# Performance work log

Hardware: AMD Instinct MI355X
Metric: run time of the kernel (lower is better)

Reference implementation:

```python
import jax, jax.numpy as jnp
import numpy as np


def _made_masks(D, H):
    # Standard MADE masks, natural ordering, param_count=2 (shift, log_scale).
    d_in = np.arange(1, D + 1)                      # input degrees 1..D
    d_h = (np.arange(H) % (D - 1)) + 1              # hidden degrees cycle 1..D-1
    d_out = np.tile(d_in, 2)                        # output degrees, 2 params per dim
    M1 = (d_h[None, :] >= d_in[:, None]).astype(np.float32)   # [D, H]
    M2 = (d_out[None, :] > d_h[:, None]).astype(np.float32)
    return jnp.asarray(M1), jnp.asarray(M2)


def setup_inputs() -> dict:
    key = jax.random.key(0)
    B, D, H = 4096, 1024, 4096
    k0, k1, k2 = jax.random.split(key, 3)
    z = jax.random.normal(k0, (B, D), dtype=jnp.float32)
    W1 = jax.random.normal(k1, (D, H), dtype=jnp.float32) * (1.0 / np.sqrt(D))
    b1 = jnp.zeros((H,), dtype=jnp.float32)
    # small init on output layer keeps exp(log_scale) well-conditioned
    W2 = jax.random.normal(k2, (H, 2 * D), dtype=jnp.float32) * (0.1 / np.sqrt(H))
    b2 = jnp.zeros((2 * D,), dtype=jnp.float32)
    permutation = jnp.arange(D, dtype=jnp.int32)
    return {"z": z, "W1": W1, "b1": b1, "W2": W2, "b2": b2, "permutation": permutation}


def reference(z, W1, b1, W2, b2, permutation):
    # IAR.forward_flow: permute -> MADE masked MLP -> split params -> affine transform -> inverse permute
    D = z.shape[1]
    H = W1.shape[1]
    M1, M2 = _made_masks(D, H)
    zp = z[:, permutation]                          # permute_data
    h = jax.nn.relu(zp @ (W1 * M1) + b1)            # [B, H]
    res = h @ (W2 * M2) + b2                        # [B, 2D]
    mu, log_s = res[:, :D], res[:, D:]              # res.split(dim_in, dim=1)
    x = zp * jnp.exp(log_s) + mu                    # affine transform, forward=True
    log_det = jnp.sum(log_s, axis=1)                # [B]
    inv = jnp.argsort(permutation)                  # inv_permute_data
    return x[:, inv], log_det
```

## Files before the change

### kernel.cpp

```cpp
#include <hip/hip_runtime.h>
#include <stdint.h>


typedef float   f32x4  __attribute__((ext_vector_type(4)));
typedef int     i32x4  __attribute__((ext_vector_type(4)));
typedef int     i32x8  __attribute__((ext_vector_type(8)));

__device__ __forceinline__ uint8_t f2fp8(float f) {
    int p = __builtin_amdgcn_cvt_pk_fp8_f32(f, 0.0f, 0, false);
    return (uint8_t)(p & 0xff);
}
__device__ __forceinline__ int8_t f2i8(float v, float s) {
    float q = rintf(v * s);
    q = fminf(fmaxf(q, -127.0f), 127.0f);
    return (int8_t)q;
}

#define GLD16(g, l)                                                          \
    __builtin_amdgcn_global_load_lds(                                        \
        (const __attribute__((address_space(1))) uint32_t*)(g),              \
        (__attribute__((address_space(3))) uint32_t*)(l), 16, 0, 0)

#define MFMA_MX(a, b, c)                                                     \
    __builtin_amdgcn_mfma_scale_f32_16x16x128_f8f6f4(                        \
        (a), (b), (c), 0, 0, 0, 0x7F7F7F7F, 0, 0x7F7F7F7F)

__global__ __launch_bounds__(256) void prep_k(
    const float* __restrict__ W1, int8_t* __restrict__ W1mT,
    const float* __restrict__ W2, uint8_t* __restrict__ W2mT,
    float* __restrict__ ws2p,
    const float* __restrict__ z, const int* __restrict__ perm,
    int8_t* __restrict__ zp, float* __restrict__ ld,
    int D, int H, int B) {
    const int bx  = blockIdx.x;
    const int tid = threadIdx.x;
    const int NB1 = (H / 64) * (D / 64);
    const int NB2 = (2 * D / 64) * (H / 64);

    if (bx < NB1) {
        __shared__ int8_t t[64][68];
        const int c0 = (bx % (H / 64)) * 64;
        const int r0 = (bx / (H / 64)) * 64;
        const int q  = tid & 15;
        const int r  = tid >> 4;

        const int fid = bx * 256 + tid;
        if (fid < B) ld[fid] = 0.0f;

#pragma unroll
        for (int rr0 = 0; rr0 < 64; rr0 += 16) {
            const int rr  = rr0 + r;
            const int row = r0 + rr;
            const float4 v4 =
                *(const float4*)&W1[(size_t)row * H + c0 + q * 4];
            const float vv[4] = {v4.x, v4.y, v4.z, v4.w};
            union { int8_t b4[4]; uint32_t u; } pk;
#pragma unroll
            for (int j = 0; j < 4; j++) {
                const int c = c0 + q * 4 + j;
                pk.b4[j] = ((c % (D - 1)) >= row) ? f2i8(vv[j], 1024.0f)
                                                  : (int8_t)0;
            }
            *(uint32_t*)&t[rr][q * 4] = pk.u;
        }
        __syncthreads();
#pragma unroll
        for (int pass = 0; pass < 2; pass++) {
            const int cc = pass * 32 + (tid >> 3);
            const int j0 = (tid & 7) * 8;
            union { int8_t b[8]; uint64_t qq; } v;
#pragma unroll
            for (int j = 0; j < 8; j++) v.b[j] = t[j0 + j][cc];
            *(uint64_t*)&W1mT[(size_t)(c0 + cc) * D + r0 + j0] = v.qq;
        }
    } else if (bx < NB1 + NB2) {
        __shared__ uint8_t t[64][68];
        const int idx = bx - NB1;
        const int c0 = (idx % (2 * D / 64)) * 64;
        const int r0 = (idx / (2 * D / 64)) * 64;
        const int q  = tid & 15;
        const int r  = tid >> 4;
        const bool second = (c0 >= D);
        const int cb = (c0 - D) >> 6;

#pragma unroll
        for (int rr0 = 0; rr0 < 64; rr0 += 16) {
            const int rr  = rr0 + r;
            const int row = r0 + rr;
            const float4 v4 =
                *(const float4*)&W2[(size_t)row * 2 * D + c0 + q * 4];
            const float vv[4] = {v4.x, v4.y, v4.z, v4.w};
            union { uint8_t b4[4]; uint32_t u; } pk;
            float s = 0.0f;
#pragma unroll
            for (int j = 0; j < 4; j++) {
                const int c = c0 + q * 4 + j;
                const bool keep = ((c % D) > (row % (D - 1)));
                pk.b4[j] = keep ? f2fp8(vv[j] * 256.0f) : (uint8_t)0;
                s += keep ? vv[j] : 0.0f;
            }
            *(uint32_t*)&t[rr][q * 4] = pk.u;
            if (second) {
#pragma unroll
                for (int o = 8; o > 0; o >>= 1) s += __shfl_down(s, o, 16);
                if (q == 0) ws2p[(size_t)cb * H + row] = s;
            }
        }
        __syncthreads();
#pragma unroll
        for (int pass = 0; pass < 2; pass++) {
            const int cc = pass * 32 + (tid >> 3);
            const int j0 = (tid & 7) * 8;
            union { uint8_t b[8]; uint64_t qq; } v;
#pragma unroll
            for (int j = 0; j < 8; j++) v.b[j] = t[j0 + j][cc];
            *(uint64_t*)&W2mT[(size_t)(c0 + cc) * H + r0 + j0] = v.qq;
        }
    } else {
        const int bp = bx - NB1 - NB2;
        const int i0 = tid * 4;
        const int4 p4 = *(const int4*)(perm + i0);
#pragma unroll
        for (int rr = 0; rr < 2; rr++) {
            const int b = bp * 2 + rr;
            const float* zr = z + (size_t)b * D;
            union { int8_t b4[4]; uint32_t u; } q;
            q.b4[0] = f2i8(zr[p4.x], 32.0f);
            q.b4[1] = f2i8(zr[p4.y], 32.0f);
            q.b4[2] = f2i8(zr[p4.z], 32.0f);
            q.b4[3] = f2i8(zr[p4.w], 32.0f);
            *(uint32_t*)&zp[(size_t)b * D + i0] = q.u;
        }
    }
}

__global__ __launch_bounds__(256) void gemm1_k(
    const int8_t* __restrict__ A, const int8_t* __restrict__ Bt,
    const float* __restrict__ bias, const float* __restrict__ ws2p,
    uint8_t* __restrict__ Cout, float* __restrict__ ld,
    int M, int N, int K) {
    __shared__ __align__(16) int8_t Alds[128 * 128];
    __shared__ __align__(16) int8_t Blds[128 * 128];
    __shared__ float pdl[128];

    const int id   = blockIdx.x;
    const int xcd  = id & 7, s = id >> 3;
    const int mb   = s & 31;
    const int nb   = xcd * 4 + (s >> 5);
    const int m0   = mb * 128;
    const int n0   = nb * 128;

    const int tid  = threadIdx.x;
    const int lane = tid & 63;
    const int w    = tid >> 6;
    const int wm   = (w & 1) * 64;
    const int wn   = (w >> 1) * 64;
    const int quad = lane >> 4;
    const int l16  = lane & 15;

    i32x4 acc[4][4];
#pragma unroll
    for (int i = 0; i < 4; i++)
#pragma unroll
        for (int j = 0; j < 4; j++) acc[i][j] = (i32x4)0;

    const int8_t* Ag[4];
    const int8_t* Bg[4];
    int8_t *Al[4], *Bl[4];
#pragma unroll
    for (int k = 0; k < 4; k++) {
        const int c  = tid + k * 256;
        const int so = ((c & 7) ^ ((c >> 3) & 7)) * 16;
        Ag[k] = A + (size_t)(m0 + (c >> 3)) * K + so;
        Bg[k] = Bt + (size_t)(n0 + (c >> 3)) * K + so;
        Al[k] = &Alds[c * 16];
        Bl[k] = &Blds[c * 16];
    }

    const int sw   = l16 & 7;
    const int arow = (wm + l16) * 128;
    const int brow = (wn + l16) * 128;

    for (int kt = 0; kt < K; kt += 128) {
        __syncthreads();
#pragma unroll
        for (int k = 0; k < 4; k++) {
            GLD16(Ag[k] + kt, Al[k]);
            GLD16(Bg[k] + kt, Bl[k]);
        }
        __syncthreads();

#pragma unroll
        for (int kh = 0; kh < 2; kh++) {
            const int pc = ((kh * 4 + quad) ^ sw) * 16;
            i32x4 af[4], bfr[4];
#pragma unroll
            for (int mi = 0; mi < 4; mi++)
                af[mi] = *(const i32x4*)&Alds[arow + mi * 16 * 128 + pc];
#pragma unroll
            for (int ni = 0; ni < 4; ni++)
                bfr[ni] = *(const i32x4*)&Blds[brow + ni * 16 * 128 + pc];
#pragma unroll
            for (int mi = 0; mi < 4; mi++)
#pragma unroll
                for (int ni = 0; ni < 4; ni++)
                    acc[mi][ni] = __builtin_amdgcn_mfma_i32_16x16x64_i8(
                        af[mi], bfr[ni], acc[mi][ni], 0, 0, 0);
        }
    }

    const float inv = 1.0f / 32768.0f;
    float bv[4], wv[4];
#pragma unroll
    for (int ni = 0; ni < 4; ni++) {
        const int col = n0 + wn + ni * 16 + l16;
        bv[ni] = bias[col];
        float sv = 0.0f;
#pragma unroll
        for (int cb = 0; cb < 16; cb++) sv += ws2p[(size_t)cb * N + col];
        wv[ni] = sv;
    }
    float pd[4][4];
#pragma unroll
    for (int mi = 0; mi < 4; mi++)
#pragma unroll
        for (int r = 0; r < 4; r++) pd[mi][r] = 0.0f;

#pragma unroll
    for (int mi = 0; mi < 4; mi++) {
        const int row = m0 + wm + mi * 16 + quad * 4;
#pragma unroll
        for (int ni = 0; ni < 4; ni++) {
            const int col = n0 + wn + ni * 16 + l16;
#pragma unroll
            for (int r = 0; r < 4; r++) {
                float v = fmaxf((float)acc[mi][ni][r] * inv + bv[ni], 0.0f);
                pd[mi][r] += v * wv[ni];
                Cout[(size_t)(row + r) * N + col] = f2fp8(v);
            }
        }
    }

#pragma unroll
    for (int off = 1; off < 16; off <<= 1)
#pragma unroll
        for (int mi = 0; mi < 4; mi++)
#pragma unroll
            for (int r = 0; r < 4; r++)
                pd[mi][r] += __shfl_xor(pd[mi][r], off, 16);

    __syncthreads();
    if ((w >> 1) == 0 && l16 == 0)
#pragma unroll
        for (int mi = 0; mi < 4; mi++)
#pragma unroll
            for (int r = 0; r < 4; r++)
                pdl[wm + mi * 16 + quad * 4 + r] = pd[mi][r];
    __syncthreads();
    if ((w >> 1) == 1 && l16 == 0)
#pragma unroll
        for (int mi = 0; mi < 4; mi++)
#pragma unroll
            for (int r = 0; r < 4; r++)
                pdl[wm + mi * 16 + quad * 4 + r] += pd[mi][r];
    __syncthreads();
    if (tid < 128) atomicAdd(&ld[m0 + tid], pdl[tid]);
}

__global__ __launch_bounds__(256) void gemm2f_k(
    const uint8_t* __restrict__ A, const uint8_t* __restrict__ Bt,
    const float* __restrict__ b2, const int* __restrict__ perm,
    const float* __restrict__ z, const float* __restrict__ ld,
    float* __restrict__ out, int B, int D, int K) {
    __shared__ __align__(16) uint8_t Alds[2][128 * 128];
    __shared__ __align__(16) uint8_t Blds[2][128 * 128];
    __shared__ float red[4];

    const int id   = blockIdx.x;
    const int nb   = id & 15;
    const int s    = id >> 4;
    const int m0   = s * 128;
    const int p0   = nb * 64;

    const int tid  = threadIdx.x;
    const int lane = tid & 63;
    const int w    = tid >> 6;
    const int wm   = (w & 1) * 64;
    const int wp   = (w >> 1) * 32;
    const int quad = lane >> 4;
    const int l16  = lane & 15;

    f32x4 acc[4][4];
#pragma unroll
    for (int i = 0; i < 4; i++)
#pragma unroll
        for (int j = 0; j < 4; j++) acc[i][j] = (f32x4)0.0f;

    const uint8_t* Ag[4];
    const uint8_t* Bg[4];
    int ldso[4];
#pragma unroll
    for (int k = 0; k < 4; k++) {
        const int c  = tid + k * 256;
        const int r  = c >> 3;
        const int so = ((c & 7) ^ (r & 7)) * 16;
        Ag[k] = A + (size_t)(m0 + r) * K + so;
        const int g = (r < 64) ? (p0 + r) : (D + p0 + (r - 64));
        Bg[k] = Bt + (size_t)g * K + so;
        ldso[k] = c * 16;
    }

    const int sw   = l16 & 7;
    const int pc0  = ((quad * 2) ^ sw) * 16;
    const int pc1  = ((quad * 2 + 1) ^ sw) * 16;

#pragma unroll
    for (int k = 0; k < 4; k++) {
        GLD16(Ag[k], &Alds[0][ldso[k]]);
        GLD16(Bg[k], &Blds[0][ldso[k]]);
    }
    __syncthreads();

    int cur = 0;
    for (int kt = 0; kt < K; kt += 128) {
        const int nxt = cur ^ 1;
        if (kt + 128 < K) {
#pragma unroll
            for (int k = 0; k < 4; k++) {
                GLD16(Ag[k] + kt + 128, &Alds[nxt][ldso[k]]);
                GLD16(Bg[k] + kt + 128, &Blds[nxt][ldso[k]]);
            }
        }
        union ABu { int4 h2[2]; i32x8 v; };
        i32x8 af[4], bfr[4];
#pragma unroll
        for (int mi = 0; mi < 4; mi++) {
            ABu t;
            const int ar = (wm + mi * 16 + l16) * 128;
            t.h2[0] = *(const int4*)&Alds[cur][ar + pc0];
            t.h2[1] = *(const int4*)&Alds[cur][ar + pc1];
            af[mi] = t.v;
        }
#pragma unroll
        for (int ni = 0; ni < 4; ni++) {
            ABu t;
            const int br = ((ni >> 1) * 64 + wp + (ni & 1) * 16 + l16) * 128;
            t.h2[0] = *(const int4*)&Blds[cur][br + pc0];
            t.h2[1] = *(const int4*)&Blds[cur][br + pc1];
            bfr[ni] = t.v;
        }
#pragma unroll
        for (int mi = 0; mi < 4; mi++)
#pragma unroll
            for (int ni = 0; ni < 4; ni++)
                acc[mi][ni] = MFMA_MX(af[mi], bfr[ni], acc[mi][ni]);
        __syncthreads();
        cur = nxt;
    }

    const float inv = 1.0f / 256.0f;
    float bmu[2], bls[2];
    int   pcv[2];
#pragma unroll
    for (int ci = 0; ci < 2; ci++) {
        const int gc = p0 + wp + ci * 16 + l16;
        bmu[ci] = b2[gc];
        bls[ci] = b2[D + gc];
        pcv[ci] = perm[gc];
    }
#pragma unroll
    for (int mi = 0; mi < 4; mi++) {
        const int row0 = m0 + wm + mi * 16 + quad * 4;
#pragma unroll
        for (int ci = 0; ci < 2; ci++) {
#pragma unroll
            for (int r = 0; r < 4; r++) {
                const size_t idx = (size_t)(row0 + r) * D + pcv[ci];
                const float mu = acc[mi][ci][r] * inv + bmu[ci];
                float ls = acc[mi][ci + 2][r] * inv + bls[ci];
                ls = fminf(fmaxf(ls, -30.0f), 30.0f);
                out[idx] = z[idx] * expf(ls) + mu;
            }
        }
    }

    if (nb == 0) {
        float bs = 0.0f;
        for (int i = tid; i < D; i += 256) bs += b2[D + i];
#pragma unroll
        for (int o = 32; o > 0; o >>= 1) bs += __shfl_down(bs, o, 64);
        if ((tid & 63) == 0) red[tid >> 6] = bs;
        __syncthreads();
        if (tid < 128)
            out[(size_t)B * D + m0 + tid] =
                ld[m0 + tid] + red[0] + red[1] + red[2] + red[3];
    }
}

extern "C" void kernel_launch(void* const* d_in, const int* in_sizes, int n_in,
                              void* d_out, int out_size, void* d_ws, size_t ws_size,
                              hipStream_t stream) {
    const float* z    = (const float*)d_in[0];
    const float* W1   = (const float*)d_in[1];
    const float* b1   = (const float*)d_in[2];
    const float* W2   = (const float*)d_in[3];
    const float* b2   = (const float*)d_in[4];
    const int*   perm = (const int*)d_in[5];
    float* out = (float*)d_out;
    char*  ws  = (char*)d_ws;

    const int D = in_sizes[5];
    const int H = in_sizes[2];
    const int B = in_sizes[0] / D;

    const size_t off_h    = 0;
    const size_t off_W2mT = off_h    + (size_t)B * H;
    const size_t off_W1mT = off_W2mT + (size_t)2 * D * H;
    const size_t off_zp   = off_W1mT + (size_t)H * D;
    const size_t off_ws2  = off_zp   + (size_t)B * D;
    const size_t off_ld   = off_ws2  + (size_t)16 * H * 4;

    uint8_t* h    = (uint8_t*)(ws + off_h);
    uint8_t* W2mT = (uint8_t*)(ws + off_W2mT);
    int8_t*  W1mT = (int8_t*)(ws + off_W1mT);
    int8_t*  zp   = (int8_t*)(ws + off_zp);
    float*   ws2p = (float*)(ws + off_ws2);
    float*   ld   = (float*)(ws + off_ld);

    const int NB1 = (H / 64) * (D / 64);
    const int NB2 = (2 * D / 64) * (H / 64);
    const int NBP = B / 2;
    prep_k<<<NB1 + NB2 + NBP, 256, 0, stream>>>(
        W1, W1mT, W2, W2mT, ws2p, z, perm, zp, ld, D, H, B);

    gemm1_k<<<(H / 128) * (B / 128), 256, 0, stream>>>(
        zp, W1mT, b1, ws2p, h, ld, B, H, D);

    gemm2f_k<<<(D / 64) * (B / 128), 256, 0, stream>>>(
        h, W2mT, b2, perm, z, ld, out, B, D, H);
}
```

Measured before the change: 178.4 us.

## Prefetch two K-tiles ahead with explicit vmcnt waits and MFMA priority

Restructures the second GEMM's main loop so two K-tiles are in flight before compute starts. It replaces __syncthreads with explicit s_waitcnt vmcnt(8) plus s_barrier so the wait covers only the older tile's loads, and refills the buffer just consumed after a barrier. It also raises wave priority around the MFMA block with s_setprio. The aim is to hide global-to-LDS latency better, at the cost of relying on hand-counted vmcnt values that must match the number of outstanding loads.

Result: faster. 172.1 us (-3.6%).

```diff
diff --git a/kernel.cpp b/kernel.cpp
--- a/kernel.cpp
+++ b/kernel.cpp
@@ -319,43 +319,56 @@
         GLD16(Ag[k], &Alds[0][ldso[k]]);
         GLD16(Bg[k], &Blds[0][ldso[k]]);
     }
-    __syncthreads();
-
-    int cur = 0;
-    for (int kt = 0; kt < K; kt += 128) {
-        const int nxt = cur ^ 1;
-        if (kt + 128 < K) {
-#pragma unroll
-            for (int k = 0; k < 4; k++) {
-                GLD16(Ag[k] + kt + 128, &Alds[nxt][ldso[k]]);
-                GLD16(Bg[k] + kt + 128, &Blds[nxt][ldso[k]]);
-            }
-        }
+#pragma unroll
+    for (int k = 0; k < 4; k++) {
+        GLD16(Ag[k] + 128, &Alds[1][ldso[k]]);
+        GLD16(Bg[k] + 128, &Blds[1][ldso[k]]);
+    }
+
+    const int NT = K / 128;
+    for (int t = 0; t < NT; ++t) {
+        if (t < NT - 1) {
+            asm volatile("s_waitcnt vmcnt(8)" ::: "memory");
+        } else {
+            asm volatile("s_waitcnt vmcnt(0)" ::: "memory");
+        }
+        asm volatile("s_barrier" ::: "memory");
+
+        const int cur = t & 1;
         union ABu { int4 h2[2]; i32x8 v; };
         i32x8 af[4], bfr[4];
 #pragma unroll
         for (int mi = 0; mi < 4; mi++) {
-            ABu t;
+            ABu tt;
             const int ar = (wm + mi * 16 + l16) * 128;
-            t.h2[0] = *(const int4*)&Alds[cur][ar + pc0];
-            t.h2[1] = *(const int4*)&Alds[cur][ar + pc1];
-            af[mi] = t.v;
+            tt.h2[0] = *(const int4*)&Alds[cur][ar + pc0];
+            tt.h2[1] = *(const int4*)&Alds[cur][ar + pc1];
+            af[mi] = tt.v;
         }
 #pragma unroll
         for (int ni = 0; ni < 4; ni++) {
-            ABu t;
+            ABu tt;
             const int br = ((ni >> 1) * 64 + wp + (ni & 1) * 16 + l16) * 128;
-            t.h2[0] = *(const int4*)&Blds[cur][br + pc0];
-            t.h2[1] = *(const int4*)&Blds[cur][br + pc1];
-            bfr[ni] = t.v;
-        }
+            tt.h2[0] = *(const int4*)&Blds[cur][br + pc0];
+            tt.h2[1] = *(const int4*)&Blds[cur][br + pc1];
+            bfr[ni] = tt.v;
+        }
+        __builtin_amdgcn_s_setprio(1);
 #pragma unroll
         for (int mi = 0; mi < 4; mi++)
 #pragma unroll
             for (int ni = 0; ni < 4; ni++)
                 acc[mi][ni] = MFMA_MX(af[mi], bfr[ni], acc[mi][ni]);
-        __syncthreads();
-        cur = nxt;
+        __builtin_amdgcn_s_setprio(0);
+
+        if (t + 2 < NT) {
+            asm volatile("s_barrier" ::: "memory");
+#pragma unroll
+            for (int k = 0; k < 4; k++) {
+                GLD16(Ag[k] + (t + 2) * 128, &Alds[cur][ldso[k]]);
+                GLD16(Bg[k] + (t + 2) * 128, &Blds[cur][ldso[k]]);
+            }
+        }
     }
 
     const float inv = 1.0f / 256.0f;
```
